# Kernel tuning notes

Hardware: AMD Instinct MI355X
Metric: run time of the kernel (lower is better)

Reference implementation:

```python
import jax, jax.numpy as jnp
import numpy as np

N_NODES = 50000
N_EDGES = 800000
F_DIM = 256
H_DIM = 256
O_DIM = 64


def spmm(edge_index, edge_weight, x):
    # sparse adj (COO) @ dense x: out[dst] += w * x[src]
    src = edge_index[0]
    dst = edge_index[1]
    msgs = edge_weight[:, None] * x[src]          # [E, D]
    return jax.ops.segment_sum(msgs, dst, num_segments=x.shape[0])


def setup_inputs() -> dict:
    key = jax.random.key(0)
    ks = jax.random.split(key, 10)
    stdv = 1.0 / np.sqrt(H_DIM)
    u = lambda k, shp: jax.random.uniform(k, shp, jnp.float32, -stdv, stdv)
    return {
        "input": jax.random.normal(ks[0], (N_NODES, F_DIM), jnp.float32),
        "edge_index": jax.random.randint(ks[1], (2, N_EDGES), 0, N_NODES, jnp.int32),
        "edge_weight": jax.random.uniform(ks[2], (N_EDGES,), jnp.float32),
        "mixture_weight": u(ks[3], (1,)),
        "hidden_weight": u(ks[4], (F_DIM, H_DIM)),
        "hidden_bias": u(ks[5], (H_DIM,)),
        "mean_weight": u(ks[6], (H_DIM, O_DIM)),
        "mean_bias": u(ks[7], (O_DIM,)),
        "log_std_weight": u(ks[8], (H_DIM, O_DIM)),
        "log_std_bias": u(ks[9], (O_DIM,)),
    }


def reference(input, edge_index, edge_weight, mixture_weight, hidden_weight,
              hidden_bias, mean_weight, mean_bias, log_std_weight, log_std_bias):
    # eval mode: dropout is identity
    # --- GCN branch ---
    support = input @ hidden_weight                       # [N, H]
    hidden_g = jax.nn.relu(spmm(edge_index, edge_weight, support) + hidden_bias)
    mean_gcn = spmm(edge_index, edge_weight, hidden_g @ mean_weight)      # [N, O]
    log_std_gcn = spmm(edge_index, edge_weight, hidden_g @ log_std_weight)
    # --- MLP branch ---
    hidden_m = jax.nn.relu(support + hidden_bias)
    mean_mlp = hidden_m @ mean_weight + mean_bias
    log_std_mlp = hidden_m @ log_std_weight + log_std_bias
    # --- mixture (note: z_mean uses raw weight, z_log_std uses sigmoid, as in source) ---
    mw = mixture_weight
    mr = jax.nn.sigmoid(mixture_weight)
    z_mean = mean_gcn * mw + mean_mlp * (1.0 - mw)
    z_log_std = log_std_gcn * mr + log_std_mlp * (1.0 - mr)
    return (z_mean, z_log_std)
```

## Files before the change

kernel.cpp:

```cpp
#include <hip/hip_runtime.h>
#include <math.h>

#define NN 50000
#define NE 800000
#define KD 256
#define OD 64
#define NCH ((NN + 255) / 256)
#define EPB 4096
#define NBLK ((NE + EPB - 1) / EPB)
#define NHT (NCH * NBLK)

#define QS 32.0f
#define IQS (1.0f / 32.0f)
#define QS2 16.0f
#define IQS2 (1.0f / 16.0f)

using bf16x8 = __attribute__((ext_vector_type(8))) short;
using f32x4  = __attribute__((ext_vector_type(4))) float;

__device__ __forceinline__ unsigned short f2b(float x) {
    union { float f; unsigned u; } c; c.f = x;
    unsigned r = (c.u + 0x7FFF + ((c.u >> 16) & 1)) >> 16;
    return (unsigned short)r;
}
__device__ __forceinline__ float b2f(unsigned short b) {
    union { unsigned u; float f; } c; c.u = ((unsigned)b) << 16;
    return c.f;
}
__device__ __forceinline__ signed char quant8(float v) {
    int q = __float2int_rn(v * QS);
    q = q > 127 ? 127 : (q < -127 ? -127 : q);
    return (signed char)q;
}
__device__ __forceinline__ unsigned quant16u(float v) {
    int q = __float2int_rn(v * QS2);
    return (unsigned)(q > 127 ? 127 : q);
}

__device__ __forceinline__ void blk_scan(int* s, int t) {
    for (int o = 1; o < 256; o <<= 1) {
        int x = (t >= o) ? s[t - o] : 0;
        __syncthreads();
        s[t] += x;
        __syncthreads();
    }
}


__global__ __launch_bounds__(256) void k_histconv(const int* __restrict__ dst,
                                                  int* __restrict__ histT,
                                                  const float* __restrict__ hw,
                                                  const float* __restrict__ mw_,
                                                  const float* __restrict__ lw,
                                                  unsigned short* __restrict__ Wht,
                                                  unsigned short* __restrict__ Wmlt) {
    __shared__ int bins[NCH];
    int t = threadIdx.x;
    if (blockIdx.x < NBLK) {
        int blk = blockIdx.x;
        if (t < NCH) bins[t] = 0;
        __syncthreads();
        int base = blk * EPB;
        #pragma unroll
        for (int i = 0; i < EPB / 256; ++i) {
            int e = base + i * 256 + t;
            if (e < NE) atomicAdd(&bins[dst[e] >> 8], 1);
        }
        __syncthreads();
        if (t < NCH) histT[t * NBLK + blk] = bins[t];
    } else {
        int idx = (blockIdx.x - NBLK) * 256 + t;
        if (idx < 256 * 256) {
            int n = idx >> 8, k = idx & 255;
            Wht[(size_t)n * 256 + k] = f2b(hw[(size_t)k * 256 + n]);
        }
        if (idx < 128 * 256) {
            int n = idx >> 8, k = idx & 255;
            float v = (n < 64) ? mw_[(size_t)k * 64 + n] : lw[(size_t)k * 64 + (n - 64)];
            Wmlt[(size_t)n * 256 + k] = f2b(v);
        }
    }
}

__global__ __launch_bounds__(256) void k_scanbins(int* __restrict__ histT,
                                                  int* __restrict__ binSum) {
    __shared__ int s[256];
    int bin = blockIdx.x, t = threadIdx.x;
    int v = (t < NBLK) ? histT[bin * NBLK + t] : 0;
    s[t] = v;
    __syncthreads();
    blk_scan(s, t);
    if (t < NBLK) histT[bin * NBLK + t] = s[t] - v;
    if (t == NBLK - 1) binSum[bin] = s[t];
}

__global__ __launch_bounds__(256) void k_bucketw(const int* __restrict__ src,
                                                 const int* __restrict__ dst,
                                                 const float* __restrict__ w,
                                                 const int* __restrict__ histT,
                                                 const int* __restrict__ binSum,
                                                 int2* __restrict__ bkt) {
    __shared__ int pre[256];
    __shared__ int cur[NCH];
    int t = threadIdx.x, blk = blockIdx.x;
    int v = (t < NCH) ? binSum[t] : 0;
    pre[t] = v;
    __syncthreads();
    blk_scan(pre, t);
    if (t < NCH) cur[t] = histT[t * NBLK + blk] + (pre[t] - v);
    __syncthreads();
    int base = blk * EPB;
    #pragma unroll
    for (int i = 0; i < EPB / 256; ++i) {
        int e = base + i * 256 + t;
        if (e < NE) {
            int d = dst[e];
            int p = atomicAdd(&cur[d >> 8], 1);
            bkt[p] = make_int2((d << 16) | src[e], __float_as_int(w[e]));
        }
    }
}

__global__ __launch_bounds__(256) void k_deg2(const int2* __restrict__ bkt,
                                              const int* __restrict__ binSum,
                                              int* __restrict__ deg,
                                              int* __restrict__ chunkSum8) {
    __shared__ int incl[256];
    __shared__ int cnt[256];
    int t = threadIdx.x, b = blockIdx.x;
    incl[t] = (t < NCH) ? binSum[t] : 0;
    cnt[t] = 0;
    __syncthreads();
    blk_scan(incl, t);
    int e0 = (b > 0) ? incl[b - 1] : 0;
    int e1 = incl[b];
    __syncthreads();
    for (int e = e0 + t; e < e1; e += 256)
        atomicAdd(&cnt[(((unsigned)bkt[e].x) >> 16) & 255], 1);
    __syncthreads();
    int node = b * 256 + t;
    int c = cnt[t];
    if (node < NN) deg[node] = c;
    __shared__ int s[256];
    s[t] = (node < NN) ? ((c + 7) & ~7) : 0;
    __syncthreads();
    for (int o = 128; o > 0; o >>= 1) {
        if (t < o) s[t] += s[t + o];
        __syncthreads();
    }
    if (t == 0) chunkSum8[b] = s[0];
}

__global__ __launch_bounds__(256) void k_place2f(const int2* __restrict__ bkt,
                                                 const int* __restrict__ binSum,
                                                 const int* __restrict__ chunkSum8,
                                                 const int* __restrict__ deg,
                                                 int* __restrict__ offsets8,
                                                 int2* __restrict__ pedge) {
    __shared__ int binc[256];
    __shared__ int cinc[256];
    __shared__ int s[256];
    __shared__ int ncur[256];
    int t = threadIdx.x, b = blockIdx.x;
    binc[t] = (t < NCH) ? binSum[t] : 0;
    __syncthreads();
    blk_scan(binc, t);
    cinc[t] = (t < NCH) ? chunkSum8[t] : 0;
    __syncthreads();
    blk_scan(cinc, t);
    int e0 = (b > 0) ? binc[b - 1] : 0;
    int e1 = binc[b];
    int chunkBase = (b > 0) ? cinc[b - 1] : 0;
    __syncthreads();
    int node = b * 256 + t;
    int dv = (node < NN) ? deg[node] : 0;
    int pv = (dv + 7) & ~7;
    s[t] = pv;
    __syncthreads();
    blk_scan(s, t);
    int excl = s[t] - pv + chunkBase;
    if (node <= NN) offsets8[node] = excl;
    ncur[t] = excl;
    __syncthreads();
    for (int e = e0 + t; e < e1; e += 256) {
        int2 v = bkt[e];
        int d = ((unsigned)v.x) >> 16;
        int p = atomicAdd(&ncur[d & 255], 1);
        pedge[p] = v;
    }
    __syncthreads();
    if (node < NN) {
        int p0 = ncur[t];
        int p1 = excl + pv;
        for (int p = p0; p < p1; ++p) pedge[p] = make_int2(0, 0);
    }
}


__global__ __launch_bounds__(256) void k_gemm1(const float* __restrict__ Ap,
                                               const unsigned short* __restrict__ Bt,
                                               signed char* __restrict__ supqOut) {
    __shared__ unsigned short As[64 * 64];
    __shared__ unsigned short Bs[128 * 64];
    const int tid = threadIdx.x;
    const int row0 = blockIdx.x * 64;
    const int n0 = blockIdx.y * 128;
    const int lane = tid & 63;
    const int w = tid >> 6, wm = w >> 1, wn = w & 1;
    const int lr = lane & 15, lg = lane >> 4;
    const int rA = tid >> 2, qA = tid & 3;
    const int rB = tid >> 1, hB = tid & 1;

    f32x4 acc[2][4] = {};

    for (int k0 = 0; k0 < KD; k0 += 64) {
        {
            int gr = row0 + rA;
            unsigned short tmp[16];
            if (gr < NN) {
                #pragma unroll
                for (int i = 0; i < 4; ++i) {
                    float4 v = *reinterpret_cast<const float4*>(
                        &Ap[(size_t)gr * KD + k0 + qA * 16 + i * 4]);
                    tmp[i * 4 + 0] = f2b(v.x); tmp[i * 4 + 1] = f2b(v.y);
                    tmp[i * 4 + 2] = f2b(v.z); tmp[i * 4 + 3] = f2b(v.w);
                }
            } else {
                #pragma unroll
                for (int i = 0; i < 16; ++i) tmp[i] = 0;
            }
            int s0 = (qA * 2) ^ (rA & 7);
            int s1 = (qA * 2 + 1) ^ (rA & 7);
            *reinterpret_cast<uint4*>(&As[rA * 64 + s0 * 8]) = *reinterpret_cast<const uint4*>(&tmp[0]);
            *reinterpret_cast<uint4*>(&As[rA * 64 + s1 * 8]) = *reinterpret_cast<const uint4*>(&tmp[8]);
        }
        {
            const unsigned short* B = Bt + (size_t)(n0 + rB) * KD + k0 + hB * 32;
            #pragma unroll
            for (int i = 0; i < 4; ++i) {
                uint4 u = *reinterpret_cast<const uint4*>(B + i * 8);
                int slot = (hB * 4 + i) ^ (rB & 7);
                *reinterpret_cast<uint4*>(&Bs[rB * 64 + slot * 8]) = u;
            }
        }
        __syncthreads();
        #pragma unroll
        for (int ks = 0; ks < 2; ++ks) {
            int slot = ks * 4 + lg;
            bf16x8 a[2], b[4];
            #pragma unroll
            for (int fm = 0; fm < 2; ++fm) {
                int ra = wm * 32 + fm * 16 + lr;
                a[fm] = *reinterpret_cast<const bf16x8*>(&As[ra * 64 + ((slot ^ (ra & 7))) * 8]);
            }
            #pragma unroll
            for (int fn = 0; fn < 4; ++fn) {
                int rb = wn * 64 + fn * 16 + lr;
                b[fn] = *reinterpret_cast<const bf16x8*>(&Bs[rb * 64 + ((slot ^ (rb & 7))) * 8]);
            }
            #pragma unroll
            for (int fm = 0; fm < 2; ++fm)
                #pragma unroll
                for (int fn = 0; fn < 4; ++fn)
                    acc[fm][fn] = __builtin_amdgcn_mfma_f32_16x16x32_bf16(a[fm], b[fn], acc[fm][fn], 0, 0, 0);
        }
        __syncthreads();
    }
    #pragma unroll
    for (int fm = 0; fm < 2; ++fm) {
        #pragma unroll
        for (int j = 0; j < 4; ++j) {
            int grow = row0 + wm * 32 + fm * 16 + lg * 4 + j;
            if (grow >= NN) continue;
            #pragma unroll
            for (int fn = 0; fn < 4; ++fn) {
                int gcol = n0 + wn * 64 + fn * 16 + lr;
                supqOut[(size_t)grow * 256 + gcol] = quant8(acc[fm][fn][j]);
            }
        }
    }
}


__global__ __launch_bounds__(256) void k_gemm2(const signed char* __restrict__ hgq,
                                               const signed char* __restrict__ supq,
                                               const unsigned short* __restrict__ Bt,
                                               const float* __restrict__ hbias,
                                               const float* __restrict__ mbias,
                                               const float* __restrict__ lbias,
                                               signed char* __restrict__ gcnq,
                                               unsigned short* __restrict__ mlpout) {
    __shared__ unsigned short As[64 * 64];
    __shared__ unsigned short Bs[128 * 64];
    const bool mlpMode = blockIdx.y != 0;
    const int tid = threadIdx.x;
    const int row0 = blockIdx.x * 64;
    const int lane = tid & 63;
    const int w = tid >> 6, wm = w >> 1, wn = w & 1;
    const int lr = lane & 15, lg = lane >> 4;
    const int rA = tid >> 2, qA = tid & 3;
    const int rB = tid >> 1, hB = tid & 1;

    f32x4 acc[2][4] = {};

    for (int k0 = 0; k0 < KD; k0 += 64) {
        {
            int gr = row0 + rA;
            unsigned short tmp[16];
            if (gr < NN) {
                signed char q[16];
                const signed char* Aq = mlpMode ? supq : hgq;
                *reinterpret_cast<uint4*>(q) =
                    *reinterpret_cast<const uint4*>(&Aq[(size_t)gr * KD + k0 + qA * 16]);
                if (mlpMode) {
                    #pragma unroll
                    for (int i = 0; i < 4; ++i) {
                        float4 hb4 = *reinterpret_cast<const float4*>(&hbias[k0 + qA * 16 + i * 4]);
                        tmp[i * 4 + 0] = f2b(fmaxf((float)q[i * 4 + 0] * IQS + hb4.x, 0.f));
                        tmp[i * 4 + 1] = f2b(fmaxf((float)q[i * 4 + 1] * IQS + hb4.y, 0.f));
                        tmp[i * 4 + 2] = f2b(fmaxf((float)q[i * 4 + 2] * IQS + hb4.z, 0.f));
                        tmp[i * 4 + 3] = f2b(fmaxf((float)q[i * 4 + 3] * IQS + hb4.w, 0.f));
                    }
                } else {
                    #pragma unroll
                    for (int i = 0; i < 16; ++i) tmp[i] = f2b((float)q[i] * IQS2);
                }
            } else {
                #pragma unroll
                for (int i = 0; i < 16; ++i) tmp[i] = 0;
            }
            int s0 = (qA * 2) ^ (rA & 7);
            int s1 = (qA * 2 + 1) ^ (rA & 7);
            *reinterpret_cast<uint4*>(&As[rA * 64 + s0 * 8]) = *reinterpret_cast<const uint4*>(&tmp[0]);
            *reinterpret_cast<uint4*>(&As[rA * 64 + s1 * 8]) = *reinterpret_cast<const uint4*>(&tmp[8]);
        }
        {
            const unsigned short* B = Bt + (size_t)rB * KD + k0 + hB * 32;
            #pragma unroll
            for (int i = 0; i < 4; ++i) {
                uint4 u = *reinterpret_cast<const uint4*>(B + i * 8);
                int slot = (hB * 4 + i) ^ (rB & 7);
                *reinterpret_cast<uint4*>(&Bs[rB * 64 + slot * 8]) = u;
            }
        }
        __syncthreads();
        #pragma unroll
        for (int ks = 0; ks < 2; ++ks) {
            int slot = ks * 4 + lg;
            bf16x8 a[2], b[4];
            #pragma unroll
            for (int fm = 0; fm < 2; ++fm) {
                int ra = wm * 32 + fm * 16 + lr;
                a[fm] = *reinterpret_cast<const bf16x8*>(&As[ra * 64 + ((slot ^ (ra & 7))) * 8]);
            }
            #pragma unroll
            for (int fn = 0; fn < 4; ++fn) {
                int rb = wn * 64 + fn * 16 + lr;
                b[fn] = *reinterpret_cast<const bf16x8*>(&Bs[rb * 64 + ((slot ^ (rb & 7))) * 8]);
            }
            #pragma unroll
            for (int fm = 0; fm < 2; ++fm)
                #pragma unroll
                for (int fn = 0; fn < 4; ++fn)
                    acc[fm][fn] = __builtin_amdgcn_mfma_f32_16x16x32_bf16(a[fm], b[fn], acc[fm][fn], 0, 0, 0);
        }
        __syncthreads();
    }
    #pragma unroll
    for (int fm = 0; fm < 2; ++fm) {
        #pragma unroll
        for (int j = 0; j < 4; ++j) {
            int grow = row0 + wm * 32 + fm * 16 + lg * 4 + j;
            if (grow >= NN) continue;
            #pragma unroll
            for (int fn = 0; fn < 4; ++fn) {
                int gcol = wn * 64 + fn * 16 + lr;
                float v = acc[fm][fn][j];
                if (mlpMode) {
                    float b = (gcol < 64) ? mbias[gcol] : lbias[gcol - 64];
                    mlpout[(size_t)grow * 128 + gcol] = f2b(v + b);
                } else {
                    gcnq[(size_t)grow * 128 + gcol] = quant8(v);
                }
            }
        }
    }
}


__global__ __launch_bounds__(256) void k_spmm1(const int* __restrict__ off8,
                                               const int2* __restrict__ pedge,
                                               const unsigned* __restrict__ supq,
                                               const float* __restrict__ bias,
                                               unsigned* __restrict__ hgq) {
    int lane = threadIdx.x & 63;
    int wid = blockIdx.x * 4 + (threadIdx.x >> 6);
    int d0 = wid * 2, d1 = d0 + 1;
    int ea = off8[d0], eA = off8[d0 + 1], eB = off8[d0 + 2];
    int eb = eA;
    float a0 = 0.f, a1 = 0.f, a2 = 0.f, a3 = 0.f;
    float c0 = 0.f, c1 = 0.f, c2 = 0.f, c3 = 0.f;
    for (; ea < eA && eb < eB; ea += 8, eb += 8) {
        int2 Ea[8], Eb[8];
        unsigned Ua[8], Ub[8];
        #pragma unroll
        for (int i = 0; i < 8; ++i) { Ea[i] = pedge[ea + i]; Eb[i] = pedge[eb + i]; }
        #pragma unroll
        for (int i = 0; i < 8; ++i) {
            Ua[i] = supq[(size_t)(Ea[i].x & 0xffff) * 64 + lane];
            Ub[i] = supq[(size_t)(Eb[i].x & 0xffff) * 64 + lane];
        }
        #pragma unroll
        for (int i = 0; i < 8; ++i) {
            float wa = __int_as_float(Ea[i].y), wb = __int_as_float(Eb[i].y);
            unsigned ua = Ua[i], ub = Ub[i];
            a0 = fmaf(wa, (float)((int)(signed char)(ua)), a0);
            a1 = fmaf(wa, (float)((int)(signed char)(ua >> 8)), a1);
            a2 = fmaf(wa, (float)((int)(signed char)(ua >> 16)), a2);
            a3 = fmaf(wa, (float)((int)(signed char)(ua >> 24)), a3);
            c0 = fmaf(wb, (float)((int)(signed char)(ub)), c0);
            c1 = fmaf(wb, (float)((int)(signed char)(ub >> 8)), c1);
            c2 = fmaf(wb, (float)((int)(signed char)(ub >> 16)), c2);
            c3 = fmaf(wb, (float)((int)(signed char)(ub >> 24)), c3);
        }
    }
    for (; ea < eA; ea += 8) {
        int2 E[8]; unsigned U[8];
        #pragma unroll
        for (int i = 0; i < 8; ++i) E[i] = pedge[ea + i];
        #pragma unroll
        for (int i = 0; i < 8; ++i) U[i] = supq[(size_t)(E[i].x & 0xffff) * 64 + lane];
        #pragma unroll
        for (int i = 0; i < 8; ++i) {
            float w = __int_as_float(E[i].y); unsigned u = U[i];
            a0 = fmaf(w, (float)((int)(signed char)(u)), a0);
            a1 = fmaf(w, (float)((int)(signed char)(u >> 8)), a1);
            a2 = fmaf(w, (float)((int)(signed char)(u >> 16)), a2);
            a3 = fmaf(w, (float)((int)(signed char)(u >> 24)), a3);
        }
    }
    for (; eb < eB; eb += 8) {
        int2 E[8]; unsigned U[8];
        #pragma unroll
        for (int i = 0; i < 8; ++i) E[i] = pedge[eb + i];
        #pragma unroll
        for (int i = 0; i < 8; ++i) U[i] = supq[(size_t)(E[i].x & 0xffff) * 64 + lane];
        #pragma unroll
        for (int i = 0; i < 8; ++i) {
            float w = __int_as_float(E[i].y); unsigned u = U[i];
            c0 = fmaf(w, (float)((int)(signed char)(u)), c0);
            c1 = fmaf(w, (float)((int)(signed char)(u >> 8)), c1);
            c2 = fmaf(w, (float)((int)(signed char)(u >> 16)), c2);
            c3 = fmaf(w, (float)((int)(signed char)(u >> 24)), c3);
        }
    }
    float4 b = *reinterpret_cast<const float4*>(&bias[lane * 4]);
    unsigned oa = quant16u(fmaxf(a0 * IQS + b.x, 0.f))
                | (quant16u(fmaxf(a1 * IQS + b.y, 0.f)) << 8)
                | (quant16u(fmaxf(a2 * IQS + b.z, 0.f)) << 16)
                | (quant16u(fmaxf(a3 * IQS + b.w, 0.f)) << 24);
    unsigned oc = quant16u(fmaxf(c0 * IQS + b.x, 0.f))
                | (quant16u(fmaxf(c1 * IQS + b.y, 0.f)) << 8)
                | (quant16u(fmaxf(c2 * IQS + b.z, 0.f)) << 16)
                | (quant16u(fmaxf(c3 * IQS + b.w, 0.f)) << 24);
    hgq[(size_t)d0 * 64 + lane] = oa;
    hgq[(size_t)d1 * 64 + lane] = oc;
}


__global__ __launch_bounds__(256) void k_spmm2(const int* __restrict__ off8,
                                               const int2* __restrict__ pedge,
                                               const unsigned short* __restrict__ gq,
                                               const unsigned short* __restrict__ mlp,
                                               const float* __restrict__ mixw,
                                               float* __restrict__ out) {
    int lane = threadIdx.x & 63;
    int wid = blockIdx.x * 4 + (threadIdx.x >> 6);
    int d0 = wid * 2, d1 = d0 + 1;
    int ea = off8[d0], eA = off8[d0 + 1], eB = off8[d0 + 2];
    int eb = eA;
    float a0 = 0.f, a1 = 0.f, c0 = 0.f, c1 = 0.f;
    for (; ea < eA && eb < eB; ea += 8, eb += 8) {
        int2 Ea[8], Eb[8];
        unsigned short Ua[8], Ub[8];
        #pragma unroll
        for (int i = 0; i < 8; ++i) { Ea[i] = pedge[ea + i]; Eb[i] = pedge[eb + i]; }
        #pragma unroll
        for (int i = 0; i < 8; ++i) {
            Ua[i] = gq[(size_t)(Ea[i].x & 0xffff) * 64 + lane];
            Ub[i] = gq[(size_t)(Eb[i].x & 0xffff) * 64 + lane];
        }
        #pragma unroll
        for (int i = 0; i < 8; ++i) {
            float wa = __int_as_float(Ea[i].y), wb = __int_as_float(Eb[i].y);
            a0 = fmaf(wa, (float)((int)(signed char)(Ua[i] & 0xff)), a0);
            a1 = fmaf(wa, (float)((int)(signed char)(Ua[i] >> 8)), a1);
            c0 = fmaf(wb, (float)((int)(signed char)(Ub[i] & 0xff)), c0);
            c1 = fmaf(wb, (float)((int)(signed char)(Ub[i] >> 8)), c1);
        }
    }
    for (; ea < eA; ea += 8) {
        int2 E[8]; unsigned short U[8];
        #pragma unroll
        for (int i = 0; i < 8; ++i) E[i] = pedge[ea + i];
        #pragma unroll
        for (int i = 0; i < 8; ++i) U[i] = gq[(size_t)(E[i].x & 0xffff) * 64 + lane];
        #pragma unroll
        for (int i = 0; i < 8; ++i) {
            float w = __int_as_float(E[i].y);
            a0 = fmaf(w, (float)((int)(signed char)(U[i] & 0xff)), a0);
            a1 = fmaf(w, (float)((int)(signed char)(U[i] >> 8)), a1);
        }
    }
    for (; eb < eB; eb += 8) {
        int2 E[8]; unsigned short U[8];
        #pragma unroll
        for (int i = 0; i < 8; ++i) E[i] = pedge[eb + i];
        #pragma unroll
        for (int i = 0; i < 8; ++i) U[i] = gq[(size_t)(E[i].x & 0xffff) * 64 + lane];
        #pragma unroll
        for (int i = 0; i < 8; ++i) {
            float w = __int_as_float(E[i].y);
            c0 = fmaf(w, (float)((int)(signed char)(U[i] & 0xff)), c0);
            c1 = fmaf(w, (float)((int)(signed char)(U[i] >> 8)), c1);
        }
    }
    float mw = mixw[0];
    float mr = 1.f / (1.f + expf(-mw));
    int c = lane * 2;
    ushort2 mu0 = reinterpret_cast<const ushort2*>(mlp)[(size_t)d0 * 64 + lane];
    ushort2 mu1 = reinterpret_cast<const ushort2*>(mlp)[(size_t)d1 * 64 + lane];
    float g00 = a0 * IQS, g01 = a1 * IQS;
    float g10 = c0 * IQS, g11 = c1 * IQS;
    if (c < 64) {
        *reinterpret_cast<float2*>(out + (size_t)d0 * OD + c) =
            make_float2(g00 * mw + b2f(mu0.x) * (1.f - mw), g01 * mw + b2f(mu0.y) * (1.f - mw));
        *reinterpret_cast<float2*>(out + (size_t)d1 * OD + c) =
            make_float2(g10 * mw + b2f(mu1.x) * (1.f - mw), g11 * mw + b2f(mu1.y) * (1.f - mw));
    } else {
        float* ol = out + (size_t)NN * OD;
        *reinterpret_cast<float2*>(ol + (size_t)d0 * OD + (c - 64)) =
            make_float2(g00 * mr + b2f(mu0.x) * (1.f - mr), g01 * mr + b2f(mu0.y) * (1.f - mr));
        *reinterpret_cast<float2*>(ol + (size_t)d1 * OD + (c - 64)) =
            make_float2(g10 * mr + b2f(mu1.x) * (1.f - mr), g11 * mr + b2f(mu1.y) * (1.f - mr));
    }
}


extern "C" void kernel_launch(void* const* d_in, const int* in_sizes, int n_in,
                              void* d_out, int out_size, void* d_ws, size_t ws_size,
                              hipStream_t stream) {
    const float* input = (const float*)d_in[0];
    const int*   ei    = (const int*)d_in[1];
    const float* ew    = (const float*)d_in[2];
    const float* mixw  = (const float*)d_in[3];
    const float* hw    = (const float*)d_in[4];
    const float* hb    = (const float*)d_in[5];
    const float* mw_   = (const float*)d_in[6];
    const float* mb    = (const float*)d_in[7];
    const float* lw    = (const float*)d_in[8];
    const float* lb    = (const float*)d_in[9];
    float* out = (float*)d_out;

    const int* src = ei;
    const int* dst = ei + NE;

    char* ws = (char*)d_ws;
    size_t off = 0;
    auto alloc = [&](size_t bytes) -> void* {
        void* p = ws + off;
        off += (bytes + 255) & ~(size_t)255;
        return p;
    };
    int*   deg      = (int*)alloc((size_t)NN * 4);
    int*   offsets8 = (int*)alloc((size_t)(NN + 2) * 4);
    int*   chunkSum8= (int*)alloc((size_t)NCH * 4);
    int*   binSum   = (int*)alloc((size_t)NCH * 4);
    int*   histT    = (int*)alloc((size_t)NHT * 4);
    int2*  bkt      = (int2*)alloc((size_t)NE * 8);
    int2*  pedge    = (int2*)alloc(((size_t)NE + 8 * NN) * 8);
    unsigned short* Wht  = (unsigned short*)alloc((size_t)256 * 256 * 2);
    unsigned short* Wmlt = (unsigned short*)alloc((size_t)128 * 256 * 2);
    signed char*    supq     = (signed char*)alloc((size_t)NN * KD);
    signed char*    hgq      = (signed char*)alloc((size_t)NN * KD);
    signed char*    gcnq     = (signed char*)alloc((size_t)NN * 128);
    unsigned short* mlp      = (unsigned short*)alloc((size_t)NN * 128 * 2);

    k_histconv<<<NBLK + 256, 256, 0, stream>>>(dst, histT, hw, mw_, lw, Wht, Wmlt);
    k_scanbins<<<NCH, 256, 0, stream>>>(histT, binSum);
    k_bucketw<<<NBLK, 256, 0, stream>>>(src, dst, ew, histT, binSum, bkt);
    k_deg2<<<NCH, 256, 0, stream>>>(bkt, binSum, deg, chunkSum8);
    k_place2f<<<NCH, 256, 0, stream>>>(bkt, binSum, chunkSum8, deg, offsets8, pedge);

    int mblk = (NN + 63) / 64;
    k_gemm1<<<dim3(mblk, 2), 256, 0, stream>>>(input, Wht, supq);
    k_spmm1<<<NN / 8, 256, 0, stream>>>(offsets8, pedge, (const unsigned*)supq, hb, (unsigned*)hgq);
    k_gemm2<<<dim3(mblk, 2), 256, 0, stream>>>(hgq, supq, Wmlt, hb, mb, lb, gcnq, mlp);
    k_spmm2<<<NN / 8, 256, 0, stream>>>(offsets8, pedge, (const unsigned short*)gcnq, mlp, mixw, out);
}
```

Before: 150.6 us.

## Fuse CSR build kernels into one cooperative kernel with grid syncs

Merges the five preprocessing kernels (histogram plus weight conversion, bin scan, bucketing, degree count, placement) into a single cooperative launch separated by grid.sync barriers. The degree counts now stay in shared memory between phases, which removes the deg buffer. This cuts four kernel launch gaps and one global round trip. In exchange, every block pays for grid-wide barriers, and the grid of about 452 blocks must fit co-resident for the cooperative launch to succeed.

Measured after the change: 343.7 us. +128.3%, slower.

```diff
diff --git a/kernel.cpp b/kernel.cpp
--- a/kernel.cpp
+++ b/kernel.cpp
@@ -1,5 +1,8 @@
 #include <hip/hip_runtime.h>
+#include <hip/hip_cooperative_groups.h>
 #include <math.h>
+
+namespace cg = cooperative_groups;
 
 #define NN 50000
 #define NE 800000
@@ -9,6 +12,7 @@
 #define EPB 4096
 #define NBLK ((NE + EPB - 1) / EPB)
 #define NHT (NCH * NBLK)
+#define CSRG (NBLK + 256)
 
 #define QS 32.0f
 #define IQS (1.0f / 32.0f)
@@ -47,29 +51,39 @@
 }
 
 
-__global__ __launch_bounds__(256) void k_histconv(const int* __restrict__ dst,
-                                                  int* __restrict__ histT,
-                                                  const float* __restrict__ hw,
-                                                  const float* __restrict__ mw_,
-                                                  const float* __restrict__ lw,
-                                                  unsigned short* __restrict__ Wht,
-                                                  unsigned short* __restrict__ Wmlt) {
-    __shared__ int bins[NCH];
-    int t = threadIdx.x;
-    if (blockIdx.x < NBLK) {
-        int blk = blockIdx.x;
-        if (t < NCH) bins[t] = 0;
-        __syncthreads();
-        int base = blk * EPB;
+__global__ __launch_bounds__(256) void k_csr(const int* __restrict__ src,
+                                             const int* __restrict__ dst,
+                                             const float* __restrict__ ew,
+                                             const float* __restrict__ hw,
+                                             const float* __restrict__ mw_,
+                                             const float* __restrict__ lw,
+                                             unsigned short* __restrict__ Wht,
+                                             unsigned short* __restrict__ Wmlt,
+                                             int* __restrict__ histT,
+                                             int* __restrict__ binSum,
+                                             int* __restrict__ chunkSum8,
+                                             int2* __restrict__ bkt,
+                                             int* __restrict__ offsets8,
+                                             int2* __restrict__ pedge) {
+    cg::grid_group grid = cg::this_grid();
+    __shared__ int sA[256];
+    __shared__ int sB[256];
+    __shared__ int cnt[256];
+    const int t = threadIdx.x, b = blockIdx.x;
+
+    if (b < NBLK) {
+        if (t < NCH) sA[t] = 0;
+        __syncthreads();
+        int base = b * EPB;
         #pragma unroll
         for (int i = 0; i < EPB / 256; ++i) {
             int e = base + i * 256 + t;
-            if (e < NE) atomicAdd(&bins[dst[e] >> 8], 1);
-        }
-        __syncthreads();
-        if (t < NCH) histT[t * NBLK + blk] = bins[t];
+            if (e < NE) atomicAdd(&sA[dst[e] >> 8], 1);
+        }
+        __syncthreads();
+        if (t < NCH) histT[t * NBLK + b] = sA[t];
     } else {
-        int idx = (blockIdx.x - NBLK) * 256 + t;
+        int idx = (b - NBLK) * 256 + t;
         if (idx < 256 * 256) {
             int n = idx >> 8, k = idx & 255;
             Wht[(size_t)n * 256 + k] = f2b(hw[(size_t)k * 256 + n]);
@@ -80,119 +94,89 @@
             Wmlt[(size_t)n * 256 + k] = f2b(v);
         }
     }
-}
-
-__global__ __launch_bounds__(256) void k_scanbins(int* __restrict__ histT,
-                                                  int* __restrict__ binSum) {
-    __shared__ int s[256];
-    int bin = blockIdx.x, t = threadIdx.x;
-    int v = (t < NBLK) ? histT[bin * NBLK + t] : 0;
-    s[t] = v;
-    __syncthreads();
-    blk_scan(s, t);
-    if (t < NBLK) histT[bin * NBLK + t] = s[t] - v;
-    if (t == NBLK - 1) binSum[bin] = s[t];
-}
-
-__global__ __launch_bounds__(256) void k_bucketw(const int* __restrict__ src,
-                                                 const int* __restrict__ dst,
-                                                 const float* __restrict__ w,
-                                                 const int* __restrict__ histT,
-                                                 const int* __restrict__ binSum,
-                                                 int2* __restrict__ bkt) {
-    __shared__ int pre[256];
-    __shared__ int cur[NCH];
-    int t = threadIdx.x, blk = blockIdx.x;
-    int v = (t < NCH) ? binSum[t] : 0;
-    pre[t] = v;
-    __syncthreads();
-    blk_scan(pre, t);
-    if (t < NCH) cur[t] = histT[t * NBLK + blk] + (pre[t] - v);
-    __syncthreads();
-    int base = blk * EPB;
-    #pragma unroll
-    for (int i = 0; i < EPB / 256; ++i) {
-        int e = base + i * 256 + t;
-        if (e < NE) {
-            int d = dst[e];
-            int p = atomicAdd(&cur[d >> 8], 1);
-            bkt[p] = make_int2((d << 16) | src[e], __float_as_int(w[e]));
-        }
-    }
-}
-
-__global__ __launch_bounds__(256) void k_deg2(const int2* __restrict__ bkt,
-                                              const int* __restrict__ binSum,
-                                              int* __restrict__ deg,
-                                              int* __restrict__ chunkSum8) {
-    __shared__ int incl[256];
-    __shared__ int cnt[256];
-    int t = threadIdx.x, b = blockIdx.x;
-    incl[t] = (t < NCH) ? binSum[t] : 0;
-    cnt[t] = 0;
-    __syncthreads();
-    blk_scan(incl, t);
-    int e0 = (b > 0) ? incl[b - 1] : 0;
-    int e1 = incl[b];
-    __syncthreads();
-    for (int e = e0 + t; e < e1; e += 256)
-        atomicAdd(&cnt[(((unsigned)bkt[e].x) >> 16) & 255], 1);
-    __syncthreads();
-    int node = b * 256 + t;
-    int c = cnt[t];
-    if (node < NN) deg[node] = c;
-    __shared__ int s[256];
-    s[t] = (node < NN) ? ((c + 7) & ~7) : 0;
-    __syncthreads();
-    for (int o = 128; o > 0; o >>= 1) {
-        if (t < o) s[t] += s[t + o];
-        __syncthreads();
-    }
-    if (t == 0) chunkSum8[b] = s[0];
-}
-
-__global__ __launch_bounds__(256) void k_place2f(const int2* __restrict__ bkt,
-                                                 const int* __restrict__ binSum,
-                                                 const int* __restrict__ chunkSum8,
-                                                 const int* __restrict__ deg,
-                                                 int* __restrict__ offsets8,
-                                                 int2* __restrict__ pedge) {
-    __shared__ int binc[256];
-    __shared__ int cinc[256];
-    __shared__ int s[256];
-    __shared__ int ncur[256];
-    int t = threadIdx.x, b = blockIdx.x;
-    binc[t] = (t < NCH) ? binSum[t] : 0;
-    __syncthreads();
-    blk_scan(binc, t);
-    cinc[t] = (t < NCH) ? chunkSum8[t] : 0;
-    __syncthreads();
-    blk_scan(cinc, t);
-    int e0 = (b > 0) ? binc[b - 1] : 0;
-    int e1 = binc[b];
-    int chunkBase = (b > 0) ? cinc[b - 1] : 0;
-    __syncthreads();
-    int node = b * 256 + t;
-    int dv = (node < NN) ? deg[node] : 0;
-    int pv = (dv + 7) & ~7;
-    s[t] = pv;
-    __syncthreads();
-    blk_scan(s, t);
-    int excl = s[t] - pv + chunkBase;
-    if (node <= NN) offsets8[node] = excl;
-    ncur[t] = excl;
-    __syncthreads();
-    for (int e = e0 + t; e < e1; e += 256) {
-        int2 v = bkt[e];
-        int d = ((unsigned)v.x) >> 16;
-        int p = atomicAdd(&ncur[d & 255], 1);
-        pedge[p] = v;
-    }
-    __syncthreads();
-    if (node < NN) {
-        int p0 = ncur[t];
-        int p1 = excl + pv;
-        for (int p = p0; p < p1; ++p) pedge[p] = make_int2(0, 0);
+    grid.sync();
+
+    if (b < NCH) {
+        int v = (t < NBLK) ? histT[b * NBLK + t] : 0;
+        sA[t] = v;
+        __syncthreads();
+        blk_scan(sA, t);
+        if (t < NBLK) histT[b * NBLK + t] = sA[t] - v;
+        if (t == NBLK - 1) binSum[b] = sA[t];
+    }
+    grid.sync();
+
+    if (b < NBLK) {
+        int v = (t < NCH) ? binSum[t] : 0;
+        sA[t] = v;
+        __syncthreads();
+        blk_scan(sA, t);
+        if (t < NCH) sB[t] = histT[t * NBLK + b] + (sA[t] - v);
+        __syncthreads();
+        int base = b * EPB;
+        #pragma unroll
+        for (int i = 0; i < EPB / 256; ++i) {
+            int e = base + i * 256 + t;
+            if (e < NE) {
+                int d = dst[e];
+                int p = atomicAdd(&sB[d >> 8], 1);
+                bkt[p] = make_int2((d << 16) | src[e], __float_as_int(ew[e]));
+            }
+        }
+    }
+    grid.sync();
+
+    int e0 = 0, e1 = 0;
+    if (b < NCH) {
+        sA[t] = (t < NCH) ? binSum[t] : 0;
+        cnt[t] = 0;
+        __syncthreads();
+        blk_scan(sA, t);
+        e0 = (b > 0) ? sA[b - 1] : 0;
+        e1 = sA[b];
+        __syncthreads();
+        for (int e = e0 + t; e < e1; e += 256)
+            atomicAdd(&cnt[(((unsigned)bkt[e].x) >> 16) & 255], 1);
+        __syncthreads();
+        int node = b * 256 + t;
+        sA[t] = (node < NN) ? ((cnt[t] + 7) & ~7) : 0;
+        __syncthreads();
+        for (int o = 128; o > 0; o >>= 1) {
+            if (t < o) sA[t] += sA[t + o];
+            __syncthreads();
+        }
+        if (t == 0) chunkSum8[b] = sA[0];
+    }
+    grid.sync();
+
+    if (b < NCH) {
+        sA[t] = (t < NCH) ? chunkSum8[t] : 0;
+        __syncthreads();
+        blk_scan(sA, t);
+        int chunkBase = (b > 0) ? sA[b - 1] : 0;
+        __syncthreads();
+        int node = b * 256 + t;
+        int dv = (node < NN) ? cnt[t] : 0;
+        int pv = (dv + 7) & ~7;
+        sA[t] = pv;
+        __syncthreads();
+        blk_scan(sA, t);
+        int excl = sA[t] - pv + chunkBase;
+        if (node <= NN) offsets8[node] = excl;
+        sB[t] = excl;
+        __syncthreads();
+        for (int e = e0 + t; e < e1; e += 256) {
+            int2 v = bkt[e];
+            int d = ((unsigned)v.x) >> 16;
+            int p = atomicAdd(&sB[d & 255], 1);
+            pedge[p] = v;
+        }
+        __syncthreads();
+        if (node < NN) {
+            int p0 = sB[t];
+            int p1 = excl + pv;
+            for (int p = p0; p < p1; ++p) pedge[p] = make_int2(0, 0);
+        }
     }
 }
 
@@ -572,7 +556,6 @@
         off += (bytes + 255) & ~(size_t)255;
         return p;
     };
-    int*   deg      = (int*)alloc((size_t)NN * 4);
     int*   offsets8 = (int*)alloc((size_t)(NN + 2) * 4);
     int*   chunkSum8= (int*)alloc((size_t)NCH * 4);
     int*   binSum   = (int*)alloc((size_t)NCH * 4);
@@ -586,11 +569,16 @@
     signed char*    gcnq     = (signed char*)alloc((size_t)NN * 128);
     unsigned short* mlp      = (unsigned short*)alloc((size_t)NN * 128 * 2);
 
-    k_histconv<<<NBLK + 256, 256, 0, stream>>>(dst, histT, hw, mw_, lw, Wht, Wmlt);
-    k_scanbins<<<NCH, 256, 0, stream>>>(histT, binSum);
-    k_bucketw<<<NBLK, 256, 0, stream>>>(src, dst, ew, histT, binSum, bkt);
-    k_deg2<<<NCH, 256, 0, stream>>>(bkt, binSum, deg, chunkSum8);
-    k_place2f<<<NCH, 256, 0, stream>>>(bkt, binSum, chunkSum8, deg, offsets8, pedge);
+    {
+        void* args[] = {
+            (void*)&src, (void*)&dst, (void*)&ew,
+            (void*)&hw, (void*)&mw_, (void*)&lw,
+            (void*)&Wht, (void*)&Wmlt,
+            (void*)&histT, (void*)&binSum, (void*)&chunkSum8,
+            (void*)&bkt, (void*)&offsets8, (void*)&pedge
+        };
+        hipLaunchCooperativeKernel((const void*)k_csr, dim3(CSRG), dim3(256), args, 0, stream);
+    }
 
     int mblk = (NN + 63) / 64;
     k_gemm1<<<dim3(mblk, 2), 256, 0, stream>>>(input, Wht, supq);
```
